# Performance work log

Measured on AMD Instinct MI355X. Metric: run time of the kernel, lower is better.

The kernel has to match this reference:

```python
import jax, jax.numpy as jnp
import numpy as np

C = 512
C8 = C // 8
B, H, W = 4, 64, 64


def _conv1x1(x, w, b):
    # x: (B, Cin, H, W), w: (Cout, Cin), b: (Cout,)
    return jnp.einsum('oi,bihw->bohw', w, x) + b[None, :, None, None]


def setup_inputs() -> dict:
    key = jax.random.key(0)
    ks = jax.random.split(key, 16)
    s = 0.02
    inp = {
        'x': jax.random.normal(ks[0], (B, C, H, W), dtype=jnp.float32),
        'wpq': jax.random.normal(ks[1], (C8, C), dtype=jnp.float32) * s,
        'bpq': jnp.zeros((C8,), jnp.float32),
        'wpk': jax.random.normal(ks[2], (C8, C), dtype=jnp.float32) * s,
        'bpk': jnp.zeros((C8,), jnp.float32),
        'wpv': jax.random.normal(ks[3], (C, C), dtype=jnp.float32) * s,
        'bpv': jnp.zeros((C,), jnp.float32),
        'wcq': jax.random.normal(ks[4], (C, C), dtype=jnp.float32) * s,
        'bcq': jnp.zeros((C,), jnp.float32),
        'wck': jax.random.normal(ks[5], (C, C), dtype=jnp.float32) * s,
        'bck': jnp.zeros((C,), jnp.float32),
        'wcv': jax.random.normal(ks[6], (C, C), dtype=jnp.float32) * s,
        'bcv': jnp.zeros((C,), jnp.float32),
        # gammas are zero-init in torch; use small nonzero values so both
        # attention branches contribute to the output numerically.
        'gpos': jax.random.normal(ks[7], (1,), dtype=jnp.float32) * 0.1,
        'gchan': jax.random.normal(ks[8], (1,), dtype=jnp.float32) * 0.1,
    }
    return inp


def reference(x, wpq, bpq, wpk, bpk, wpv, bpv, wcq, bcq, wck, bck, wcv, bcv, gpos, gchan):
    b, c, h, w = x.shape
    n = h * w
    # ---- position attention ----
    pos_q = _conv1x1(x, wpq, bpq).reshape(b, C8, n)           # (b, C/8, N)
    pos_k = _conv1x1(x, wpk, bpk).reshape(b, C8, n)           # (b, C/8, N)
    pos_v = _conv1x1(x, wpv, bpv).reshape(b, c, n)            # (b, C, N)
    pos_attn = jax.nn.softmax(jnp.einsum('bcq,bck->bqk', pos_q, pos_k), axis=-1)  # (b, N, N)
    pos_out = jnp.einsum('bck,bqk->bcq', pos_v, pos_attn).reshape(b, c, h, w)
    pos_out = gpos * pos_out + x
    # ---- channel attention ----
    chan_q = _conv1x1(pos_out, wcq, bcq).reshape(b, c, n)
    chan_k = _conv1x1(pos_out, wck, bck).reshape(b, c, n)
    chan_v = _conv1x1(pos_out, wcv, bcv).reshape(b, c, n)
    chan_attn = jax.nn.softmax(jnp.einsum('bin,bjn->bij', chan_q, chan_k), axis=-1)  # (b, C, C)
    chan_out = jnp.einsum('bij,bjn->bin', chan_attn, chan_v).reshape(b, c, h, w)
    return gchan * chan_out + pos_out
```

## Files before the change

kernel.cpp:

```cpp
#include <hip/hip_runtime.h>
#include <hip/hip_bf16.h>
#include <math.h>

typedef __bf16 bf16;
typedef __attribute__((ext_vector_type(8))) __bf16 bf16x8;
typedef __attribute__((ext_vector_type(4))) __bf16 bf16x4;
typedef __attribute__((ext_vector_type(4))) float f32x4;

#define DEVI static __device__ __forceinline__

DEVI int swzb(int row, int ch) { return ((ch ^ (row & 7)) << 4); }

DEVI void gl_lds16(const void* g, void* l) {
  __builtin_amdgcn_global_load_lds(
      (const __attribute__((address_space(1))) unsigned int*)g,
      (__attribute__((address_space(3))) unsigned int*)l, 16, 0, 0);
}

template<int N> DEVI void wait_vm() {
  if constexpr (N == 0) asm volatile("s_waitcnt vmcnt(0)" ::: "memory");
  else if constexpr (N == 4) asm volatile("s_waitcnt vmcnt(4)" ::: "memory");
  else if constexpr (N == 6) asm volatile("s_waitcnt vmcnt(6)" ::: "memory");
  else if constexpr (N == 8) asm volatile("s_waitcnt vmcnt(8)" ::: "memory");
}
DEVI void sbar() {
  __builtin_amdgcn_sched_barrier(0);
  __builtin_amdgcn_s_barrier();
  __builtin_amdgcn_sched_barrier(0);
}

__global__ __launch_bounds__(256) void prep_weights(
    const float* __restrict__ wpq, const float* __restrict__ wpk,
    const float* __restrict__ wpv, const float* __restrict__ wcq,
    const float* __restrict__ wck, const float* __restrict__ wcv,
    const float* __restrict__ bpq, const float* __restrict__ bpk,
    bf16* __restrict__ wqk, bf16* __restrict__ wpvb, bf16* __restrict__ wcqb,
    bf16* __restrict__ wckb, bf16* __restrict__ wcvT, float* __restrict__ bqk)
{
  int i = blockIdx.x * 256 + threadIdx.x;
  switch (blockIdx.y) {
    case 0: if (i < 64*512)  wqk[i]          = (bf16)wpq[i]; break;
    case 1: if (i < 64*512)  wqk[64*512 + i] = (bf16)wpk[i]; break;
    case 2: if (i < 512*512) wpvb[i] = (bf16)wpv[i]; break;
    case 3: if (i < 512*512) wcqb[i] = (bf16)wcq[i]; break;
    case 4: if (i < 512*512) wckb[i] = (bf16)wck[i]; break;
    case 5: if (i < 512*512) { int t = i >> 9, j = i & 511; wcvT[i] = (bf16)wcv[j*512 + t]; } break;
    case 6: if (i < 64) bqk[i] = bpq[i]; else if (i < 128) bqk[i] = bpk[i - 64]; break;
  }
}

__global__ __launch_bounds__(256) void transpose_x(const float* __restrict__ x, bf16* __restrict__ xbT)
{
  __shared__ float t[32][33];
  int b = blockIdx.z, n0 = blockIdx.x * 32, c0 = blockIdx.y * 32;
  int tx = threadIdx.x & 31, ty = threadIdx.x >> 5;
#pragma unroll
  for (int i = 0; i < 4; ++i)
    t[ty + 8*i][tx] = x[((size_t)b*512 + c0 + ty + 8*i)*4096 + n0 + tx];
  __syncthreads();
#pragma unroll
  for (int i = 0; i < 4; ++i)
    xbT[((size_t)b*4096 + n0 + ty + 8*i)*512 + c0 + tx] = (bf16)t[tx][ty + 8*i];
}

struct GemmP {
  const bf16* A; const bf16* Bt; void* C;
  long aS, bS;
  long cSbytes;
  int lda, ldb, ldc, K;
  const float* biasM; const float* biasN;
  const float* e_bq; const float* e_v; const float* e_u; const float* e_bk; float e_nn;
  long vS, uS;
  const float* gchan; const float* Abv; const bf16* Pres; long abvS, presS;
};

template<int BM, int BN, int BIAS, int EPI>
__global__ __launch_bounds__(256) void gemm_k(GemmP p)
{
  constexpr int QF = BM / 32;
  constexpr int CF = BN / 32;
  constexpr int NBUF = (BM + BN <= 192) ? 3 : 2;
  constexpr int LOADS = (BM + BN) / 32;
  __shared__ __align__(16) char sa[NBUF][BM * 128];
  __shared__ __align__(16) char sb[NBUF][BN * 128];
  const int tid = threadIdx.x, lane = tid & 63, w = tid >> 6;
  const int g = lane >> 4, l15 = lane & 15;
  const int bm = blockIdx.x * BM, bn = blockIdx.y * BN, bz = blockIdx.z;
  const bf16* A  = p.A  + (size_t)bz * p.aS;
  const bf16* Bt = p.Bt + (size_t)bz * p.bS;
  char* Cb = (char*)p.C + (size_t)bz * p.cSbytes;
  const int wm = (w & 1) * (BM / 2), wn = (w >> 1) * (BN / 2);
  const int srow = tid >> 3, sch = tid & 7;

  f32x4 acc[QF][CF];
#pragma unroll
  for (int i = 0; i < QF; ++i)
#pragma unroll
    for (int j = 0; j < CF; ++j) acc[i][j] = f32x4{0.f, 0.f, 0.f, 0.f};

  auto stage = [&](int k0, int bi) {
#pragma unroll
    for (int it = 0; it < BM / 32; ++it) {
      int r = it * 32 + srow;
      gl_lds16(A + (size_t)(bm + r) * p.lda + k0 + ((sch ^ (r & 7)) * 8),
               sa[bi] + (it * 32 + w * 8) * 128);
    }
#pragma unroll
    for (int it = 0; it < BN / 32; ++it) {
      int r = it * 32 + srow;
      gl_lds16(Bt + (size_t)(bn + r) * p.ldb + k0 + ((sch ^ (r & 7)) * 8),
               sb[bi] + (it * 32 + w * 8) * 128);
    }
  };
  auto compute = [&](int bi) {
#pragma unroll
    for (int kc = 0; kc < 2; ++kc) {
      bf16x8 af[QF], bfr[CF];
#pragma unroll
      for (int qf = 0; qf < QF; ++qf) {
        int row = wm + 16 * qf + l15;
        af[qf] = *(const bf16x8*)(sa[bi] + row * 128 + swzb(row, g + 4 * kc));
      }
#pragma unroll
      for (int cf = 0; cf < CF; ++cf) {
        int row = wn + 16 * cf + l15;
        bfr[cf] = *(const bf16x8*)(sb[bi] + row * 128 + swzb(row, g + 4 * kc));
      }
      __builtin_amdgcn_s_setprio(1);
#pragma unroll
      for (int qf = 0; qf < QF; ++qf)
#pragma unroll
        for (int cf = 0; cf < CF; ++cf)
          acc[qf][cf] = __builtin_amdgcn_mfma_f32_16x16x32_bf16(af[qf], bfr[cf], acc[qf][cf], 0, 0, 0);
      __builtin_amdgcn_s_setprio(0);
    }
  };

  const int nk = p.K >> 6;
  if constexpr (NBUF == 3) {
    stage(0, 0);
    if (nk > 1) { stage(64, 1); wait_vm<LOADS>(); } else wait_vm<0>();
    sbar();
    int bi = 0;
    for (int t = 0; t < nk; ++t) {
      int b2 = bi + 2; if (b2 >= 3) b2 -= 3;
      if (t + 2 < nk) stage((t + 2) << 6, b2);
      compute(bi);
      if (t + 1 < nk) {
        if (t + 2 < nk) wait_vm<LOADS>(); else wait_vm<0>();
        sbar();
      }
      if (++bi == 3) bi = 0;
    }
  } else {
    stage(0, 0);
    __syncthreads();
    for (int t = 0; t < nk; ++t) {
      const int cur = t & 1;
      if (t + 1 < nk) stage((t + 1) << 6, cur ^ 1);
      compute(cur);
      __syncthreads();
    }
  }

  float gc = 0.f;
  const float* AbvB = nullptr; const bf16* PresB = nullptr;
  const float* eV = nullptr; const float* eU = nullptr;
  if (EPI == 3) { gc = p.gchan[0]; AbvB = p.Abv + (size_t)bz * p.abvS; PresB = p.Pres + (size_t)bz * p.presS; }
  if (EPI == 2) { eV = p.e_v + (size_t)bz * p.vS; eU = p.e_u + (size_t)bz * p.uS; }

#pragma unroll
  for (int qf = 0; qf < QF; ++qf)
#pragma unroll
    for (int cf = 0; cf < CF; ++cf)
#pragma unroll
      for (int r = 0; r < 4; ++r) {
        int m = bm + wm + 16 * qf + 4 * g + r;
        int n = bn + wn + 16 * cf + l15;
        float v = acc[qf][cf][r];
        if (BIAS == 1) v += p.biasM[m];
        if (BIAS == 2) v += p.biasN[n];
        size_t idx = (size_t)m * p.ldc + n;
        if (EPI == 0) ((bf16*)Cb)[idx] = (bf16)v;
        else if (EPI == 1) ((float*)Cb)[idx] = v;
        else if (EPI == 2) {
          v += p.e_bq[m] * eV[n] + eU[m] * p.e_bk[n] + p.e_nn * p.e_bq[m] * p.e_bk[n];
          ((float*)Cb)[idx] = v;
        } else {
          v = gc * (v + AbvB[m]) + (float)PresB[idx];
          ((float*)Cb)[idx] = v;
        }
      }
}

__global__ __launch_bounds__(512, 4) void flash_pos(
    const bf16* __restrict__ QKT, const bf16* __restrict__ Vv,
    const float* __restrict__ x, const float* __restrict__ gpos,
    bf16* __restrict__ Pb, bf16* __restrict__ PTb)
{
  extern __shared__ char sm[];
  float* Och  = (float*)sm;
  float* lsum = (float*)(sm + 34816);

  const int tid = threadIdx.x, lane = tid & 63, w = tid >> 6;
  const int g = lane >> 4, l15 = lane & 15;
  const int wq = w & 3;
  const int wh = w >> 2;
  const int phys = blockIdx.x;
  const int b  = (phys & 7) >> 1;
  const int ch = phys & 1;
  const int q0 = (phys >> 3) << 6;
  const int c0 = ch << 8;

  const bf16* QKTb = QKT + (size_t)b * 4096 * 128;
  const bf16* Vb   = Vv  + (size_t)b * 512 * 4096;

  const bf16* qrow = QKTb + (size_t)(q0 + 16 * wq + l15) * 128;
  bf16x8 qa0 = *(const bf16x8*)(qrow + 8 * g);
  bf16x8 qa1 = *(const bf16x8*)(qrow + 32 + 8 * g);

  f32x4 acc[4][2];
#pragma unroll
  for (int i = 0; i < 4; ++i) { acc[i][0] = f32x4{0.f,0.f,0.f,0.f}; acc[i][1] = f32x4{0.f,0.f,0.f,0.f}; }
  f32x4 l_r = f32x4{0.f, 0.f, 0.f, 0.f};

  const int srow = tid >> 3, sch = tid & 7;
  const bf16* Ksrc = QKTb + (size_t)srow * 128 + 64 + ((sch ^ (srow & 7)) * 8);
  const bf16* vb0 = Vb + (size_t)(c0 + 32 * w + l15) * 4096 + g * 8;
  const bf16* vb1 = vb0 + (size_t)16 * 4096;

  bf16x8 vA[2][2], vB[2][2];

  auto subiter = [&](int koff, int ktn, bf16x8 (&vC)[2][2], bf16x8 (&vN)[2][2]) {
    char* Kcur = sm + koff;
    char* Knext = sm + (koff ^ 8192);
    char* Pcur = sm + 16384 + koff;
    gl_lds16(Ksrc + (size_t)ktn * 8192, Knext + w * 1024);
    __builtin_amdgcn_sched_barrier(0);
#pragma unroll
    for (int kc = 0; kc < 2; ++kc) {
      vN[kc][0] = *(const bf16x8*)(vb0 + ktn * 64 + kc * 32);
      vN[kc][1] = *(const bf16x8*)(vb1 + ktn * 64 + kc * 32);
    }
    f32x4 s0 = f32x4{0.f,0.f,0.f,0.f}, s1 = f32x4{0.f,0.f,0.f,0.f};
    {
      const int r0 = 32 * wh + l15, r1 = r0 + 16;
      bf16x8 k00 = *(const bf16x8*)(Kcur + r0 * 128 + swzb(r0, g));
      bf16x8 k01 = *(const bf16x8*)(Kcur + r0 * 128 + swzb(r0, g + 4));
      bf16x8 k10 = *(const bf16x8*)(Kcur + r1 * 128 + swzb(r1, g));
      bf16x8 k11 = *(const bf16x8*)(Kcur + r1 * 128 + swzb(r1, g + 4));
      s0 = __builtin_amdgcn_mfma_f32_16x16x32_bf16(qa0, k00, s0, 0, 0, 0);
      s0 = __builtin_amdgcn_mfma_f32_16x16x32_bf16(qa1, k01, s0, 0, 0, 0);
      s1 = __builtin_amdgcn_mfma_f32_16x16x32_bf16(qa0, k10, s1, 0, 0, 0);
      s1 = __builtin_amdgcn_mfma_f32_16x16x32_bf16(qa1, k11, s1, 0, 0, 0);
    }
#pragma unroll
    for (int r = 0; r < 4; ++r) {
      float e0 = __expf(s0[r]), e1 = __expf(s1[r]);
      l_r[r] += e0 + e1;
      int row = 16 * wq + 4 * g + r;
      int ca = 32 * wh + l15, cb = ca + 16;
      *(bf16*)(Pcur + row * 128 + (((ca >> 3) ^ (row & 7)) << 4) + ((ca & 7) * 2)) = (bf16)e0;
      *(bf16*)(Pcur + row * 128 + (((cb >> 3) ^ (row & 7)) << 4) + ((cb & 7) * 2)) = (bf16)e1;
    }
    asm volatile("s_waitcnt vmcnt(4) lgkmcnt(0)" ::: "memory");
    sbar();
    __builtin_amdgcn_s_setprio(1);
#pragma unroll
    for (int kc = 0; kc < 2; ++kc)
#pragma unroll
      for (int qf = 0; qf < 4; ++qf) {
        int row = 16 * qf + l15;
        bf16x8 ap = *(const bf16x8*)(Pcur + row * 128 + swzb(row, g + 4 * kc));
        acc[qf][0] = __builtin_amdgcn_mfma_f32_16x16x32_bf16(ap, vC[kc][0], acc[qf][0], 0, 0, 0);
        acc[qf][1] = __builtin_amdgcn_mfma_f32_16x16x32_bf16(ap, vC[kc][1], acc[qf][1], 0, 0, 0);
      }
    __builtin_amdgcn_s_setprio(0);
  };

  gl_lds16(Ksrc, sm + w * 1024);
  __builtin_amdgcn_sched_barrier(0);
#pragma unroll
  for (int kc = 0; kc < 2; ++kc) {
    vA[kc][0] = *(const bf16x8*)(vb0 + kc * 32);
    vA[kc][1] = *(const bf16x8*)(vb1 + kc * 32);
  }
  asm volatile("s_waitcnt vmcnt(4)" ::: "memory");
  sbar();

  for (int t = 0; t < 64; t += 2) {
    subiter(0,    (t + 1) & 63, vA, vB);
    subiter(8192, (t + 2) & 63, vB, vA);
  }
  asm volatile("s_waitcnt vmcnt(0) lgkmcnt(0)" ::: "memory");
  sbar();

#pragma unroll
  for (int off = 1; off < 16; off <<= 1) {
#pragma unroll
    for (int r = 0; r < 4; ++r) l_r[r] += __shfl_xor(l_r[r], off);
  }
  if (l15 == 0)
#pragma unroll
    for (int r = 0; r < 4; ++r) lsum[wh * 64 + 16 * wq + 4 * g + r] = l_r[r];
  __syncthreads();

  const float gp = gpos[0];
  for (int j = 0; j < 2; ++j) {
    if ((w >> 2) == j) {
#pragma unroll
      for (int qf = 0; qf < 4; ++qf) {
        float inv[4];
#pragma unroll
        for (int r = 0; r < 4; ++r) {
          int qi = 16 * qf + 4 * g + r;
          inv[r] = gp / (lsum[qi] + lsum[64 + qi]);
        }
#pragma unroll
        for (int cf = 0; cf < 2; ++cf) {
          int cl = 32 * (w & 3) + 16 * cf + l15;
#pragma unroll
          for (int r = 0; r < 4; ++r)
            Och[cl * 68 + 16 * qf + 4 * g + r] = acc[qf][cf][r] * inv[r];
        }
      }
    }
    __syncthreads();
    {
      int cl = tid >> 2, qs = (tid & 3) * 16;
      int cg = c0 + 128 * j + cl;
      const float* xr = x + ((size_t)b * 512 + cg) * 4096 + q0 + qs;
      float* och = Och + cl * 68 + qs;
      float tmp[16];
#pragma unroll
      for (int i = 0; i < 16; ++i) { tmp[i] = och[i] + xr[i]; och[i] = tmp[i]; }
      bf16x8 o0, o1;
#pragma unroll
      for (int i = 0; i < 8; ++i) { o0[i] = (bf16)tmp[i]; o1[i] = (bf16)tmp[i + 8]; }
      bf16* pr = Pb + ((size_t)b * 512 + cg) * 4096 + q0 + qs;
      *(bf16x8*)pr = o0; *(bf16x8*)(pr + 8) = o1;
    }
    __syncthreads();
    {
      int q = tid >> 3, cs = (tid & 7) * 16;
      float tmp[16];
#pragma unroll
      for (int i = 0; i < 16; ++i) tmp[i] = Och[(cs + i) * 68 + q];
      bf16x8 o0, o1;
#pragma unroll
      for (int i = 0; i < 8; ++i) { o0[i] = (bf16)tmp[i]; o1[i] = (bf16)tmp[i + 8]; }
      bf16* pt = PTb + ((size_t)b * 4096 + q0 + q) * 512 + c0 + 128 * j + cs;
      *(bf16x8*)pt = o0; *(bf16x8*)(pt + 8) = o1;
    }
    __syncthreads();
  }
}

__global__ __launch_bounds__(256) void row_sum(const bf16* __restrict__ Pb, float* __restrict__ r)
{
  int wid = blockIdx.x * 4 + (threadIdx.x >> 6);
  int lane = threadIdx.x & 63;
  const bf16* row = Pb + (size_t)wid * 4096;
  float s = 0.f;
#pragma unroll
  for (int i = 0; i < 8; ++i) {
    bf16x8 v = ((const bf16x8*)row)[lane + 64 * i];
#pragma unroll
    for (int j = 0; j < 8; ++j) s += (float)v[j];
  }
#pragma unroll
  for (int off = 1; off < 64; off <<= 1) s += __shfl_xor(s, off);
  if (lane == 0) r[wid] = s;
}

__global__ __launch_bounds__(256) void uv_kernel(
    const float* __restrict__ wcq, const float* __restrict__ wck,
    const float* __restrict__ r, float* __restrict__ u, float* __restrict__ v)
{
  int b = blockIdx.z;
  int i = blockIdx.x * 256 + threadIdx.x;
  const float* rb = r + b * 512;
  const float* wrow = (blockIdx.y ? wck : wcq) + (size_t)i * 512;
  float s = 0.f;
  for (int t = 0; t < 512; ++t) s += wrow[t] * rb[t];
  (blockIdx.y ? v : u)[b * 512 + i] = s;
}

__global__ __launch_bounds__(256) void softmax_chan(
    const float* __restrict__ L, const float* __restrict__ bcv,
    bf16* __restrict__ Ab, float* __restrict__ Abv)
{
  int b = blockIdx.z;
  int i = blockIdx.x * 4 + (threadIdx.x >> 6);
  int lane = threadIdx.x & 63;
  const float* row = L + ((size_t)b * 512 + i) * 512;
  f32x4 v0 = ((const f32x4*)row)[lane];
  f32x4 v1 = ((const f32x4*)row)[lane + 64];
  float mx = fmaxf(fmaxf(fmaxf(v0[0], v0[1]), fmaxf(v0[2], v0[3])),
                   fmaxf(fmaxf(v1[0], v1[1]), fmaxf(v1[2], v1[3])));
#pragma unroll
  for (int off = 1; off < 64; off <<= 1) mx = fmaxf(mx, __shfl_xor(mx, off));
  float e[8]; float s = 0.f;
#pragma unroll
  for (int k = 0; k < 4; ++k) { e[k] = __expf(v0[k] - mx); s += e[k]; }
#pragma unroll
  for (int k = 0; k < 4; ++k) { e[4 + k] = __expf(v1[k] - mx); s += e[4 + k]; }
#pragma unroll
  for (int off = 1; off < 64; off <<= 1) s += __shfl_xor(s, off);
  float inv = 1.f / s;
  bf16x4 a0, a1;
  const f32x4 bv0 = ((const f32x4*)bcv)[lane];
  const f32x4 bv1 = ((const f32x4*)bcv)[lane + 64];
  float pb = 0.f;
#pragma unroll
  for (int k = 0; k < 4; ++k) {
    float p0 = e[k] * inv, p1 = e[4 + k] * inv;
    a0[k] = (bf16)p0; a1[k] = (bf16)p1;
    pb += p0 * bv0[k] + p1 * bv1[k];
  }
  bf16* arow = Ab + ((size_t)b * 512 + i) * 512;
  *(bf16x4*)(arow + 4 * lane) = a0;
  *(bf16x4*)(arow + 256 + 4 * lane) = a1;
#pragma unroll
  for (int off = 1; off < 64; off <<= 1) pb += __shfl_xor(pb, off);
  if (lane == 0) Abv[b * 512 + i] = pb;
}

extern "C" void kernel_launch(void* const* d_in, const int* in_sizes, int n_in,
                              void* d_out, int out_size, void* d_ws, size_t ws_size,
                              hipStream_t stream)
{
  const float* x    = (const float*)d_in[0];
  const float* wpq  = (const float*)d_in[1];
  const float* bpq  = (const float*)d_in[2];
  const float* wpk  = (const float*)d_in[3];
  const float* bpk  = (const float*)d_in[4];
  const float* wpv  = (const float*)d_in[5];
  const float* bpv  = (const float*)d_in[6];
  const float* wcq  = (const float*)d_in[7];
  const float* bcq  = (const float*)d_in[8];
  const float* wck  = (const float*)d_in[9];
  const float* bck  = (const float*)d_in[10];
  const float* wcv  = (const float*)d_in[11];
  const float* bcv  = (const float*)d_in[12];
  const float* gpos = (const float*)d_in[13];
  const float* gch  = (const float*)d_in[14];
  float* out = (float*)d_out;

  char* ws = (char*)d_ws;
  size_t off = 0;
  auto alloc = [&](size_t bytes) -> char* {
    char* p = ws + off; off = (off + bytes + 255) & ~(size_t)255; return p;
  };
  bf16*  xbT  = (bf16*)alloc(4UL * 4096 * 512 * 2);
  bf16*  QKT  = (bf16*)alloc(4UL * 4096 * 128 * 2);
  bf16*  V    = (bf16*)alloc(4UL * 512 * 4096 * 2);
  bf16*  Pb   = (bf16*)alloc(4UL * 512 * 4096 * 2);
  bf16*  PTb  = (bf16*)alloc(4UL * 4096 * 512 * 2);
  bf16*  G    = (bf16*)alloc(4UL * 512 * 512 * 2);
  bf16*  M1   = (bf16*)alloc(4UL * 512 * 512 * 2);
  float* Lws  = (float*)alloc(4UL * 512 * 512 * 4);
  bf16*  Ab   = (bf16*)alloc(4UL * 512 * 512 * 2);
  bf16*  B2   = (bf16*)alloc(4UL * 512 * 512 * 2);
  bf16*  wqk  = (bf16*)alloc(128UL * 512 * 2);
  bf16*  wpvb = (bf16*)alloc(512UL * 512 * 2);
  bf16*  wcqb = (bf16*)alloc(512UL * 512 * 2);
  bf16*  wckb = (bf16*)alloc(512UL * 512 * 2);
  bf16*  wcvT = (bf16*)alloc(512UL * 512 * 2);
  float* bqk  = (float*)alloc(128 * 4);
  float* rws  = (float*)alloc(4UL * 512 * 4);
  float* uws  = (float*)alloc(4UL * 512 * 4);
  float* vws  = (float*)alloc(4UL * 512 * 4);
  float* Abv  = (float*)alloc(4UL * 512 * 4);
  if (off > ws_size) return;

  prep_weights<<<dim3(1024, 7, 1), 256, 0, stream>>>(wpq, wpk, wpv, wcq, wck, wcv,
                                                     bpq, bpk, wqk, wpvb, wcqb, wckb, wcvT, bqk);
  transpose_x<<<dim3(128, 16, 4), 256, 0, stream>>>(x, xbT);

  GemmP p{};
  p = GemmP{};
  p.A = xbT; p.aS = 4096L * 512; p.lda = 512;
  p.Bt = wqk; p.bS = 0; p.ldb = 512;
  p.C = QKT; p.cSbytes = 4096L * 128 * 2; p.ldc = 128;
  p.K = 512; p.biasN = bqk;
  gemm_k<128, 64, 2, 0><<<dim3(32, 2, 4), 256, 0, stream>>>(p);

  p = GemmP{};
  p.A = wpvb; p.aS = 0; p.lda = 512;
  p.Bt = xbT; p.bS = 4096L * 512; p.ldb = 512;
  p.C = V; p.cSbytes = 512L * 4096 * 2; p.ldc = 4096;
  p.K = 512; p.biasM = bpv;
  gemm_k<128, 128, 1, 0><<<dim3(4, 32, 4), 256, 0, stream>>>(p);

  flash_pos<<<dim3(512, 1, 1), 512, 35328, stream>>>(QKT, V, x, gpos, Pb, PTb);

  p = GemmP{};
  p.A = Pb; p.aS = 512L * 4096; p.lda = 4096;
  p.Bt = Pb; p.bS = 512L * 4096; p.ldb = 4096;
  p.C = G; p.cSbytes = 512L * 512 * 2; p.ldc = 512;
  p.K = 4096;
  gemm_k<64, 64, 0, 0><<<dim3(8, 8, 4), 256, 0, stream>>>(p);

  row_sum<<<dim3(512, 1, 1), 256, 0, stream>>>(Pb, rws);
  uv_kernel<<<dim3(2, 2, 4), 256, 0, stream>>>(wcq, wck, rws, uws, vws);

  p = GemmP{};
  p.A = wcqb; p.aS = 0; p.lda = 512;
  p.Bt = G; p.bS = 512L * 512; p.ldb = 512;
  p.C = M1; p.cSbytes = 512L * 512 * 2; p.ldc = 512;
  p.K = 512;
  gemm_k<64, 64, 0, 0><<<dim3(8, 8, 4), 256, 0, stream>>>(p);

  p = GemmP{};
  p.A = M1; p.aS = 512L * 512; p.lda = 512;
  p.Bt = wckb; p.bS = 0; p.ldb = 512;
  p.C = Lws; p.cSbytes = 512L * 512 * 4; p.ldc = 512;
  p.K = 512;
  p.e_bq = bcq; p.e_v = vws; p.vS = 512; p.e_u = uws; p.uS = 512; p.e_bk = bck; p.e_nn = 4096.f;
  gemm_k<64, 64, 0, 2><<<dim3(8, 8, 4), 256, 0, stream>>>(p);

  softmax_chan<<<dim3(128, 1, 4), 256, 0, stream>>>(Lws, bcv, Ab, Abv);

  p = GemmP{};
  p.A = Ab; p.aS = 512L * 512; p.lda = 512;
  p.Bt = wcvT; p.bS = 0; p.ldb = 512;
  p.C = B2; p.cSbytes = 512L * 512 * 2; p.ldc = 512;
  p.K = 512;
  gemm_k<64, 64, 0, 0><<<dim3(8, 8, 4), 256, 0, stream>>>(p);

  p = GemmP{};
  p.A = B2; p.aS = 512L * 512; p.lda = 512;
  p.Bt = PTb; p.bS = 4096L * 512; p.ldb = 512;
  p.C = out; p.cSbytes = 512L * 4096 * 4; p.ldc = 4096;
  p.K = 512;
  p.gchan = gch; p.Abv = Abv; p.abvS = 512; p.Pres = Pb; p.presS = 512L * 4096;
  gemm_k<128, 128, 0, 3><<<dim3(4, 32, 4), 256, 0, stream>>>(p);
}
```

Before: 304.2 us.

## Stage V tiles through LDS via async global_load_lds instead of register prefetch

In the position-attention flash kernel, V is now loaded into a swizzled LDS tile with async direct-to-LDS loads, and MFMA operands are read from LDS. Previously each wave prefetched V directly into registers, double-buffered. The P buffer becomes single-buffered and the loop gains an extra full wait and barrier per iteration before the next V tile is issued. This cuts VGPR use and makes the V loads more coalesced, but LDS grows to about 57 KB, which may lower occupancy. The V load is also no longer overlapped with compute.

```diff
diff --git a/kernel.cpp b/kernel.cpp
--- a/kernel.cpp
+++ b/kernel.cpp
@@ -199,8 +199,10 @@
     bf16* __restrict__ Pb, bf16* __restrict__ PTb)
 {
   extern __shared__ char sm[];
+  char* Vlds = sm + 16384;
+  char* Plds = sm + 49152;
   float* Och  = (float*)sm;
-  float* lsum = (float*)(sm + 34816);
+  float* lsum = (float*)(sm + 57344);
 
   const int tid = threadIdx.x, lane = tid & 63, w = tid >> 6;
   const int g = lane >> 4, l15 = lane & 15;
@@ -226,22 +228,23 @@
 
   const int srow = tid >> 3, sch = tid & 7;
   const bf16* Ksrc = QKTb + (size_t)srow * 128 + 64 + ((sch ^ (srow & 7)) * 8);
-  const bf16* vb0 = Vb + (size_t)(c0 + 32 * w + l15) * 4096 + g * 8;
-  const bf16* vb1 = vb0 + (size_t)16 * 4096;
-
-  bf16x8 vA[2][2], vB[2][2];
-
-  auto subiter = [&](int koff, int ktn, bf16x8 (&vC)[2][2], bf16x8 (&vN)[2][2]) {
-    char* Kcur = sm + koff;
-    char* Knext = sm + (koff ^ 8192);
-    char* Pcur = sm + 16384 + koff;
+
+  gl_lds16(Ksrc, sm + w * 1024);
+#pragma unroll
+  for (int it = 0; it < 4; ++it) {
+    int r = it * 64 + srow;
+    gl_lds16(Vb + (size_t)(c0 + r) * 4096 + ((sch ^ (r & 7)) * 8),
+             Vlds + (it * 64 + w * 8) * 128);
+  }
+  asm volatile("s_waitcnt vmcnt(0)" ::: "memory");
+  sbar();
+
+  for (int t = 0; t < 64; ++t) {
+    const char* Kcur = sm + ((t & 1) << 13);
+    char* Knext = sm + (((t + 1) & 1) << 13);
+    const int ktn = (t + 1) & 63;
     gl_lds16(Ksrc + (size_t)ktn * 8192, Knext + w * 1024);
     __builtin_amdgcn_sched_barrier(0);
-#pragma unroll
-    for (int kc = 0; kc < 2; ++kc) {
-      vN[kc][0] = *(const bf16x8*)(vb0 + ktn * 64 + kc * 32);
-      vN[kc][1] = *(const bf16x8*)(vb1 + ktn * 64 + kc * 32);
-    }
     f32x4 s0 = f32x4{0.f,0.f,0.f,0.f}, s1 = f32x4{0.f,0.f,0.f,0.f};
     {
       const int r0 = 32 * wh + l15, r1 = r0 + 16;
@@ -249,10 +252,12 @@
       bf16x8 k01 = *(const bf16x8*)(Kcur + r0 * 128 + swzb(r0, g + 4));
       bf16x8 k10 = *(const bf16x8*)(Kcur + r1 * 128 + swzb(r1, g));
       bf16x8 k11 = *(const bf16x8*)(Kcur + r1 * 128 + swzb(r1, g + 4));
+      __builtin_amdgcn_s_setprio(1);
       s0 = __builtin_amdgcn_mfma_f32_16x16x32_bf16(qa0, k00, s0, 0, 0, 0);
       s0 = __builtin_amdgcn_mfma_f32_16x16x32_bf16(qa1, k01, s0, 0, 0, 0);
       s1 = __builtin_amdgcn_mfma_f32_16x16x32_bf16(qa0, k10, s1, 0, 0, 0);
       s1 = __builtin_amdgcn_mfma_f32_16x16x32_bf16(qa1, k11, s1, 0, 0, 0);
+      __builtin_amdgcn_s_setprio(0);
     }
 #pragma unroll
     for (int r = 0; r < 4; ++r) {
@@ -260,37 +265,34 @@
       l_r[r] += e0 + e1;
       int row = 16 * wq + 4 * g + r;
       int ca = 32 * wh + l15, cb = ca + 16;
-      *(bf16*)(Pcur + row * 128 + (((ca >> 3) ^ (row & 7)) << 4) + ((ca & 7) * 2)) = (bf16)e0;
-      *(bf16*)(Pcur + row * 128 + (((cb >> 3) ^ (row & 7)) << 4) + ((cb & 7) * 2)) = (bf16)e1;
-    }
-    asm volatile("s_waitcnt vmcnt(4) lgkmcnt(0)" ::: "memory");
+      *(bf16*)(Plds + row * 128 + (((ca >> 3) ^ (row & 7)) << 4) + ((ca & 7) * 2)) = (bf16)e0;
+      *(bf16*)(Plds + row * 128 + (((cb >> 3) ^ (row & 7)) << 4) + ((cb & 7) * 2)) = (bf16)e1;
+    }
+    asm volatile("s_waitcnt vmcnt(1) lgkmcnt(0)" ::: "memory");
     sbar();
     __builtin_amdgcn_s_setprio(1);
 #pragma unroll
-    for (int kc = 0; kc < 2; ++kc)
+    for (int kc = 0; kc < 2; ++kc) {
+      const int vra = 32 * w + l15, vrb = vra + 16;
+      bf16x8 v0 = *(const bf16x8*)(Vlds + vra * 128 + swzb(vra, g + 4 * kc));
+      bf16x8 v1 = *(const bf16x8*)(Vlds + vrb * 128 + swzb(vrb, g + 4 * kc));
 #pragma unroll
       for (int qf = 0; qf < 4; ++qf) {
         int row = 16 * qf + l15;
-        bf16x8 ap = *(const bf16x8*)(Pcur + row * 128 + swzb(row, g + 4 * kc));
-        acc[qf][0] = __builtin_amdgcn_mfma_f32_16x16x32_bf16(ap, vC[kc][0], acc[qf][0], 0, 0, 0);
-        acc[qf][1] = __builtin_amdgcn_mfma_f32_16x16x32_bf16(ap, vC[kc][1], acc[qf][1], 0, 0, 0);
+        bf16x8 ap = *(const bf16x8*)(Plds + row * 128 + swzb(row, g + 4 * kc));
+        acc[qf][0] = __builtin_amdgcn_mfma_f32_16x16x32_bf16(ap, v0, acc[qf][0], 0, 0, 0);
+        acc[qf][1] = __builtin_amdgcn_mfma_f32_16x16x32_bf16(ap, v1, acc[qf][1], 0, 0, 0);
       }
+    }
     __builtin_amdgcn_s_setprio(0);
-  };
-
-  gl_lds16(Ksrc, sm + w * 1024);
-  __builtin_amdgcn_sched_barrier(0);
-#pragma unroll
-  for (int kc = 0; kc < 2; ++kc) {
-    vA[kc][0] = *(const bf16x8*)(vb0 + kc * 32);
-    vA[kc][1] = *(const bf16x8*)(vb1 + kc * 32);
-  }
-  asm volatile("s_waitcnt vmcnt(4)" ::: "memory");
-  sbar();
-
-  for (int t = 0; t < 64; t += 2) {
-    subiter(0,    (t + 1) & 63, vA, vB);
-    subiter(8192, (t + 2) & 63, vB, vA);
+    asm volatile("s_waitcnt vmcnt(0) lgkmcnt(0)" ::: "memory");
+    sbar();
+#pragma unroll
+    for (int it = 0; it < 4; ++it) {
+      int r = it * 64 + srow;
+      gl_lds16(Vb + (size_t)(c0 + r) * 4096 + ktn * 64 + ((sch ^ (r & 7)) * 8),
+               Vlds + (it * 64 + w * 8) * 128);
+    }
   }
   asm volatile("s_waitcnt vmcnt(0) lgkmcnt(0)" ::: "memory");
   sbar();
@@ -493,7 +495,7 @@
   p.K = 512; p.biasM = bpv;
   gemm_k<128, 128, 1, 0><<<dim3(4, 32, 4), 256, 0, stream>>>(p);
 
-  flash_pos<<<dim3(512, 1, 1), 512, 35328, stream>>>(QKT, V, x, gpos, Pb, PTb);
+  flash_pos<<<dim3(512, 1, 1), 512, 57856, stream>>>(QKT, V, x, gpos, Pb, PTb);
 
   p = GemmP{};
   p.A = Pb; p.aS = 512L * 4096; p.lda = 4096;
```

Measured after the change: 269.6 us. -11.4%, faster.
